# Kernel optimization log

Measured on AMD Instinct MI355X. Metric: run time of the kernel, lower is better.

## Reference

```python
import jax, jax.numpy as jnp
import numpy as np

EMB = 1024
HEADS = 16
BLOCK = 128


def setup_inputs() -> dict:
    key = jax.random.key(0)
    k1, k2, k3 = jax.random.split(key, 3)
    B, T, C = 4, 4096, EMB
    x = jax.random.normal(k1, (B, T, C), dtype=jnp.float32)
    # Linear weights stored as [in, out] (i.e. torch W.T); qkv has no bias.
    W_qkv = jax.random.normal(k2, (C, 3 * C), dtype=jnp.float32) * 0.02
    W_proj = jax.random.normal(k3, (C, C), dtype=jnp.float32) * 0.02
    b_proj = jnp.zeros((C,), dtype=jnp.float32)
    return {"x": x, "W_qkv": W_qkv, "W_proj": W_proj, "b_proj": b_proj}


def reference(x, W_qkv, W_proj, b_proj):
    # Dropout is inference-mode identity.
    B, T, C = x.shape
    H, D, BS = HEADS, C // HEADS, BLOCK
    nb = T // BS  # number of local blocks
    qkv = x @ W_qkv  # [B,T,3C]
    q, k, v = jnp.split(qkv, 3, axis=-1)
    # [B, nb, BS, H, D] -- each block attends only within itself
    q = q.reshape(B, nb, BS, H, D)
    k = k.reshape(B, nb, BS, H, D)
    v = v.reshape(B, nb, BS, H, D)
    scores = jnp.einsum("bnqhd,bnkhd->bnhqk", q, k) / jnp.sqrt(jnp.float32(D))
    # is_decoder: causal tril within each diagonal block (tril[i:end, i:end])
    tril = jnp.tril(jnp.ones((BS, BS), dtype=bool))
    scores = jnp.where(tril, scores, -jnp.inf)
    # faithful to original: stable exp, then divide by (sum + 1e-6)
    scores = scores - jnp.max(scores, axis=-1, keepdims=True)
    e = jnp.exp(scores)
    p = e / (jnp.sum(e, axis=-1, keepdims=True) + 1e-6)
    out = jnp.einsum("bnhqk,bnkhd->bnqhd", p, v).reshape(B, T, C)
    return out @ W_proj + b_proj
```

## Files before the change

### kernel.cpp

```cpp
#include <hip/hip_runtime.h>
#include <hip/hip_bf16.h>
#include <math.h>


typedef __bf16 bf16_t;
typedef __bf16 bf16x8 __attribute__((ext_vector_type(8)));
typedef float  f32x4  __attribute__((ext_vector_type(4)));

typedef const __attribute__((address_space(1))) void* gptr_t;
typedef __attribute__((address_space(3))) void* lptr_t;

__global__ __launch_bounds__(256) void cvt_f32_bf16(const float* __restrict__ in,
                                                    bf16_t* __restrict__ out, size_t n) {
    size_t stride = (size_t)gridDim.x * blockDim.x * 4;
    for (size_t i = ((size_t)blockIdx.x * blockDim.x + threadIdx.x) * 4; i < n; i += stride) {
        float4 v = *(const float4*)(in + i);
        bf16_t t[4];
        t[0] = (bf16_t)v.x; t[1] = (bf16_t)v.y; t[2] = (bf16_t)v.z; t[3] = (bf16_t)v.w;
        *(uint2*)(out + i) = *(uint2*)t;
    }
}

__global__ __launch_bounds__(256) void transpose_cvt(const float* __restrict__ in,
                                                     bf16_t* __restrict__ out, int K, int N) {
    __shared__ float tile[32][33];
    const int tx = threadIdx.x & 31, ty = threadIdx.x >> 5;
    const int bx = blockIdx.x, by = blockIdx.y;
    #pragma unroll
    for (int i = 0; i < 4; i++) {
        const int k = by * 32 + ty + i * 8;
        tile[ty + i * 8][tx] = in[(size_t)k * N + bx * 32 + tx];
    }
    __syncthreads();
    #pragma unroll
    for (int i = 0; i < 4; i++) {
        const int n = bx * 32 + ty + i * 8;
        out[(size_t)n * K + by * 32 + tx] = (bf16_t)tile[tx][ty + i * 8];
    }
}

template <bool BF16_OUT, bool BIAS>
__global__ __launch_bounds__(256) void gemm_bt(const bf16_t* __restrict__ A,
                                               const bf16_t* __restrict__ Bt,
                                               void* __restrict__ Cout,
                                               const float* __restrict__ bias,
                                               int M, int N, int K) {
    __shared__ bf16_t As[2][128 * 32];
    __shared__ bf16_t Bs[2][128 * 32];

    const int bn = blockIdx.x, bm = blockIdx.y;
    const int tid = threadIdx.x;
    const int lane = tid & 63, wave = tid >> 6;
    const int wm = wave >> 1, wn = wave & 1;
    const int quad = lane >> 4, l16 = lane & 15;

    const bf16_t* Ab = A  + (size_t)bm * 128 * K;
    const bf16_t* Bb = Bt + (size_t)bn * 128 * K;

    f32x4 acc[4][4];
    for (int i = 0; i < 4; i++)
        for (int j = 0; j < 4; j++)
            acc[i][j] = (f32x4){0.f, 0.f, 0.f, 0.f};

    const int srow = lane >> 2;
    const int scb  = (lane & 3) * 16;

    for (int k0 = 0; k0 < K; k0 += 64) {
        #pragma unroll
        for (int half = 0; half < 2; half++) {
            #pragma unroll
            for (int i = 0; i < 2; i++) {
                const int s = wave * 2 + i;
                const int row = s * 16 + srow;
                const int kk = k0 + half * 32;
                __builtin_amdgcn_global_load_lds(
                    (gptr_t)((const char*)(Ab + (size_t)row * K + kk) + scb),
                    (lptr_t)&As[half][s * 512], 16, 0, 0);
                __builtin_amdgcn_global_load_lds(
                    (gptr_t)((const char*)(Bb + (size_t)row * K + kk) + scb),
                    (lptr_t)&Bs[half][s * 512], 16, 0, 0);
            }
        }
        __syncthreads();

        #pragma unroll
        for (int half = 0; half < 2; half++) {
            bf16x8 af[4], bf[4];
            #pragma unroll
            for (int mr = 0; mr < 4; mr++)
                af[mr] = *(const bf16x8*)&As[half][(wm * 64 + mr * 16 + l16) * 32 + quad * 8];
            #pragma unroll
            for (int nr = 0; nr < 4; nr++)
                bf[nr] = *(const bf16x8*)&Bs[half][(wn * 64 + nr * 16 + l16) * 32 + quad * 8];
            #pragma unroll
            for (int mr = 0; mr < 4; mr++)
                #pragma unroll
                for (int nr = 0; nr < 4; nr++)
                    acc[mr][nr] = __builtin_amdgcn_mfma_f32_16x16x32_bf16(af[mr], bf[nr], acc[mr][nr], 0, 0, 0);
        }
        __syncthreads();
    }

    #pragma unroll
    for (int mr = 0; mr < 4; mr++) {
        #pragma unroll
        for (int nr = 0; nr < 4; nr++) {
            const int gcol = bn * 128 + wn * 64 + nr * 16 + l16;
            #pragma unroll
            for (int reg = 0; reg < 4; reg++) {
                const int grow = bm * 128 + wm * 64 + mr * 16 + quad * 4 + reg;
                float v = acc[mr][nr][reg];
                if (BIAS) v += bias[gcol];
                if (BF16_OUT)
                    ((bf16_t*)Cout)[(size_t)grow * N + gcol] = (bf16_t)v;
                else
                    ((float*)Cout)[(size_t)grow * N + gcol] = v;
            }
        }
    }
}

__global__ __launch_bounds__(256, 3) void attn_kernel(const bf16_t* __restrict__ qkv,
                                                      bf16_t* __restrict__ attn_out) {
    __shared__ __align__(16) char smem[54272];
    bf16_t* qs = (bf16_t*)smem;
    bf16_t* ks = (bf16_t*)(smem + 18432);
    bf16_t* vT = (bf16_t*)(smem + 36864);
    bf16_t* ps = (bf16_t*)smem;

    const int tid = threadIdx.x;
    const int lane = tid & 63, wave = tid >> 6;
    const int quad = lane >> 4, l16 = lane & 15;

    const int bid = blockIdx.x;
    const int h = bid & 15;
    const int blk = (bid >> 4) & 31;
    const int b = bid >> 9;
    const int row0 = (b * 32 + blk) * 128;
    const int LDQ = 3072;

    for (int t = tid; t < 128 * 8; t += 256) {
        const int r = t >> 3;
        const int c = (t & 7) * 8;
        const bf16_t* src = qkv + (size_t)(row0 + r) * LDQ + h * 64;
        *(uint4*)&qs[r * 72 + c] = *(const uint4*)(src + c);
        *(uint4*)&ks[r * 72 + c] = *(const uint4*)(src + 1024 + c);
        bf16x8 vv = *(const bf16x8*)(src + 2048 + c);
        #pragma unroll
        for (int j = 0; j < 8; j++)
            vT[(c + j) * 136 + r] = vv[j];
    }
    __syncthreads();

    f32x4 sfrag[2][8];
    for (int mr = 0; mr < 2; mr++)
        for (int nc = 0; nc < 8; nc++)
            sfrag[mr][nc] = (f32x4){0.f, 0.f, 0.f, 0.f};

    #pragma unroll
    for (int ksl = 0; ksl < 2; ksl++) {
        bf16x8 aq[2], bk[8];
        #pragma unroll
        for (int mr = 0; mr < 2; mr++)
            aq[mr] = *(const bf16x8*)&qs[(wave * 32 + mr * 16 + l16) * 72 + ksl * 32 + quad * 8];
        #pragma unroll
        for (int nc = 0; nc < 8; nc++)
            bk[nc] = *(const bf16x8*)&ks[(nc * 16 + l16) * 72 + ksl * 32 + quad * 8];
        #pragma unroll
        for (int mr = 0; mr < 2; mr++)
            #pragma unroll
            for (int nc = 0; nc < 8; nc++)
                sfrag[mr][nc] = __builtin_amdgcn_mfma_f32_16x16x32_bf16(aq[mr], bk[nc], sfrag[mr][nc], 0, 0, 0);
    }

    #pragma unroll
    for (int mr = 0; mr < 2; mr++) {
        #pragma unroll
        for (int nc = 0; nc < 8; nc++) {
            #pragma unroll
            for (int reg = 0; reg < 4; reg++) {
                const int row = wave * 32 + mr * 16 + quad * 4 + reg;
                const int col = nc * 16 + l16;
                float s = sfrag[mr][nc][reg] * 0.125f;
                if (col > row) s = -INFINITY;
                sfrag[mr][nc][reg] = s;
            }
        }
    }

    #pragma unroll
    for (int mr = 0; mr < 2; mr++) {
        #pragma unroll
        for (int reg = 0; reg < 4; reg++) {
            float m = -INFINITY;
            #pragma unroll
            for (int nc = 0; nc < 8; nc++) m = fmaxf(m, sfrag[mr][nc][reg]);
            #pragma unroll
            for (int off = 1; off < 16; off <<= 1) m = fmaxf(m, __shfl_xor(m, off));
            float sum = 0.f;
            #pragma unroll
            for (int nc = 0; nc < 8; nc++) {
                float e = __expf(sfrag[mr][nc][reg] - m);
                sfrag[mr][nc][reg] = e;
                sum += e;
            }
            #pragma unroll
            for (int off = 1; off < 16; off <<= 1) sum += __shfl_xor(sum, off);
            const float inv = 1.0f / (sum + 1e-6f);
            #pragma unroll
            for (int nc = 0; nc < 8; nc++) sfrag[mr][nc][reg] *= inv;
        }
    }

    __syncthreads();

    #pragma unroll
    for (int mr = 0; mr < 2; mr++)
        #pragma unroll
        for (int nc = 0; nc < 8; nc++)
            #pragma unroll
            for (int reg = 0; reg < 4; reg++) {
                const int row = wave * 32 + mr * 16 + quad * 4 + reg;
                const int col = nc * 16 + l16;
                ps[row * 136 + col] = (bf16_t)sfrag[mr][nc][reg];
            }
    __syncthreads();

    f32x4 oacc[2][4];
    for (int mr = 0; mr < 2; mr++)
        for (int nd = 0; nd < 4; nd++)
            oacc[mr][nd] = (f32x4){0.f, 0.f, 0.f, 0.f};

    #pragma unroll
    for (int ksl = 0; ksl < 4; ksl++) {
        bf16x8 ap[2];
        #pragma unroll
        for (int mr = 0; mr < 2; mr++)
            ap[mr] = *(const bf16x8*)&ps[(wave * 32 + mr * 16 + l16) * 136 + ksl * 32 + quad * 8];
        #pragma unroll
        for (int nd = 0; nd < 4; nd++) {
            bf16x8 bv = *(const bf16x8*)&vT[(nd * 16 + l16) * 136 + ksl * 32 + quad * 8];
            #pragma unroll
            for (int mr = 0; mr < 2; mr++)
                oacc[mr][nd] = __builtin_amdgcn_mfma_f32_16x16x32_bf16(ap[mr], bv, oacc[mr][nd], 0, 0, 0);
        }
    }

    #pragma unroll
    for (int mr = 0; mr < 2; mr++)
        #pragma unroll
        for (int nd = 0; nd < 4; nd++)
            #pragma unroll
            for (int reg = 0; reg < 4; reg++) {
                const int row = row0 + wave * 32 + mr * 16 + quad * 4 + reg;
                const int col = h * 64 + nd * 16 + l16;
                attn_out[(size_t)row * 1024 + col] = (bf16_t)oacc[mr][nd][reg];
            }
}

extern "C" void kernel_launch(void* const* d_in, const int* in_sizes, int n_in,
                              void* d_out, int out_size, void* d_ws, size_t ws_size,
                              hipStream_t stream) {
    const float* x     = (const float*)d_in[0];
    const float* Wqkv  = (const float*)d_in[1];
    const float* Wproj = (const float*)d_in[2];
    const float* bproj = (const float*)d_in[3];

    const int M = 16384, C = 1024, N1 = 3072;

    char* ws = (char*)d_ws;
    bf16_t* xb     = (bf16_t*)(ws);
    bf16_t* wqkvT  = (bf16_t*)(ws + 33554432);
    bf16_t* wprojT = (bf16_t*)(ws + 39845888);
    bf16_t* qkvb   = (bf16_t*)(ws + 41943040);
    bf16_t* attnb  = (bf16_t*)(ws + 142606336);

    cvt_f32_bf16<<<8192, 256, 0, stream>>>(x, xb, (size_t)M * C);
    transpose_cvt<<<dim3(N1 / 32, C / 32), 256, 0, stream>>>(Wqkv, wqkvT, C, N1);
    transpose_cvt<<<dim3(C / 32, C / 32), 256, 0, stream>>>(Wproj, wprojT, C, C);

    gemm_bt<true, false><<<dim3(N1 / 128, M / 128), 256, 0, stream>>>(
        xb, wqkvT, (void*)qkvb, nullptr, M, N1, C);

    attn_kernel<<<2048, 256, 0, stream>>>(qkvb, attnb);

    gemm_bt<false, true><<<dim3(C / 128, M / 128), 256, 0, stream>>>(
        attnb, wprojT, d_out, bproj, M, C, C);
}
```

Before: 350.7 us.

## Skip causally masked tiles in local attention and balance rows across waves

Each wave now owns two 16-row groups paired as g and 7-g, so causal work is spread evenly across the four waves. The QK^T and PV MFMA loops skip key/value tiles that lie entirely above the causal diagonal. This cuts roughly half of the attention matrix multiplies, at the cost of wave-uniform branching inside unrolled loops. Masked tiles stay at zero, are set to -inf and exp to zero, so the result is unchanged.

```diff
diff --git a/kernel.cpp b/kernel.cpp
--- a/kernel.cpp
+++ b/kernel.cpp
@@ -139,6 +139,9 @@
     const int row0 = (b * 32 + blk) * 128;
     const int LDQ = 3072;
 
+    const int wu = __builtin_amdgcn_readfirstlane(wave);
+    const int g0 = wu, g1 = 7 - wu;
+
     for (int t = tid; t < 128 * 8; t += 256) {
         const int r = t >> 3;
         const int c = (t & 7) * 8;
@@ -159,27 +162,27 @@
 
     #pragma unroll
     for (int ksl = 0; ksl < 2; ksl++) {
-        bf16x8 aq[2], bk[8];
-        #pragma unroll
-        for (int mr = 0; mr < 2; mr++)
-            aq[mr] = *(const bf16x8*)&qs[(wave * 32 + mr * 16 + l16) * 72 + ksl * 32 + quad * 8];
-        #pragma unroll
-        for (int nc = 0; nc < 8; nc++)
-            bk[nc] = *(const bf16x8*)&ks[(nc * 16 + l16) * 72 + ksl * 32 + quad * 8];
-        #pragma unroll
-        for (int mr = 0; mr < 2; mr++)
-            #pragma unroll
-            for (int nc = 0; nc < 8; nc++)
-                sfrag[mr][nc] = __builtin_amdgcn_mfma_f32_16x16x32_bf16(aq[mr], bk[nc], sfrag[mr][nc], 0, 0, 0);
-    }
-
-    #pragma unroll
-    for (int mr = 0; mr < 2; mr++) {
+        bf16x8 aq0 = *(const bf16x8*)&qs[(g0 * 16 + l16) * 72 + ksl * 32 + quad * 8];
+        bf16x8 aq1 = *(const bf16x8*)&qs[(g1 * 16 + l16) * 72 + ksl * 32 + quad * 8];
         #pragma unroll
         for (int nc = 0; nc < 8; nc++) {
+            if (nc <= g1) {
+                bf16x8 bk = *(const bf16x8*)&ks[(nc * 16 + l16) * 72 + ksl * 32 + quad * 8];
+                sfrag[1][nc] = __builtin_amdgcn_mfma_f32_16x16x32_bf16(aq1, bk, sfrag[1][nc], 0, 0, 0);
+                if (nc <= g0)
+                    sfrag[0][nc] = __builtin_amdgcn_mfma_f32_16x16x32_bf16(aq0, bk, sfrag[0][nc], 0, 0, 0);
+            }
+        }
+    }
+
+    #pragma unroll
+    for (int mr = 0; mr < 2; mr++) {
+        const int g = mr ? g1 : g0;
+        #pragma unroll
+        for (int nc = 0; nc < 8; nc++) {
             #pragma unroll
             for (int reg = 0; reg < 4; reg++) {
-                const int row = wave * 32 + mr * 16 + quad * 4 + reg;
+                const int row = g * 16 + quad * 4 + reg;
                 const int col = nc * 16 + l16;
                 float s = sfrag[mr][nc][reg] * 0.125f;
                 if (col > row) s = -INFINITY;
@@ -215,15 +218,15 @@
     __syncthreads();
 
     #pragma unroll
-    for (int mr = 0; mr < 2; mr++)
+    for (int mr = 0; mr < 2; mr++) {
+        const int g = mr ? g1 : g0;
+        const int rbase = g * 16 + quad * 4;
         #pragma unroll
         for (int nc = 0; nc < 8; nc++)
             #pragma unroll
-            for (int reg = 0; reg < 4; reg++) {
-                const int row = wave * 32 + mr * 16 + quad * 4 + reg;
-                const int col = nc * 16 + l16;
-                ps[row * 136 + col] = (bf16_t)sfrag[mr][nc][reg];
-            }
+            for (int reg = 0; reg < 4; reg++)
+                ps[(rbase + reg) * 136 + nc * 16 + l16] = (bf16_t)sfrag[mr][nc][reg];
+    }
     __syncthreads();
 
     f32x4 oacc[2][4];
@@ -231,31 +234,38 @@
         for (int nd = 0; nd < 4; nd++)
             oacc[mr][nd] = (f32x4){0.f, 0.f, 0.f, 0.f};
 
+    const int s0 = g0 >> 1, s1 = g1 >> 1;
     #pragma unroll
     for (int ksl = 0; ksl < 4; ksl++) {
-        bf16x8 ap[2];
-        #pragma unroll
-        for (int mr = 0; mr < 2; mr++)
-            ap[mr] = *(const bf16x8*)&ps[(wave * 32 + mr * 16 + l16) * 136 + ksl * 32 + quad * 8];
+        if (ksl <= s1) {
+            bf16x8 ap1 = *(const bf16x8*)&ps[(g1 * 16 + l16) * 136 + ksl * 32 + quad * 8];
+            bf16x8 ap0;
+            const bool use0 = (ksl <= s0);
+            if (use0)
+                ap0 = *(const bf16x8*)&ps[(g0 * 16 + l16) * 136 + ksl * 32 + quad * 8];
+            #pragma unroll
+            for (int nd = 0; nd < 4; nd++) {
+                bf16x8 bv = *(const bf16x8*)&vT[(nd * 16 + l16) * 136 + ksl * 32 + quad * 8];
+                oacc[1][nd] = __builtin_amdgcn_mfma_f32_16x16x32_bf16(ap1, bv, oacc[1][nd], 0, 0, 0);
+                if (use0)
+                    oacc[0][nd] = __builtin_amdgcn_mfma_f32_16x16x32_bf16(ap0, bv, oacc[0][nd], 0, 0, 0);
+            }
+        }
+    }
+
+    #pragma unroll
+    for (int mr = 0; mr < 2; mr++) {
+        const int g = mr ? g1 : g0;
         #pragma unroll
         for (int nd = 0; nd < 4; nd++) {
-            bf16x8 bv = *(const bf16x8*)&vT[(nd * 16 + l16) * 136 + ksl * 32 + quad * 8];
-            #pragma unroll
-            for (int mr = 0; mr < 2; mr++)
-                oacc[mr][nd] = __builtin_amdgcn_mfma_f32_16x16x32_bf16(ap[mr], bv, oacc[mr][nd], 0, 0, 0);
-        }
-    }
-
-    #pragma unroll
-    for (int mr = 0; mr < 2; mr++)
-        #pragma unroll
-        for (int nd = 0; nd < 4; nd++)
             #pragma unroll
             for (int reg = 0; reg < 4; reg++) {
-                const int row = row0 + wave * 32 + mr * 16 + quad * 4 + reg;
+                const int row = row0 + g * 16 + quad * 4 + reg;
                 const int col = h * 64 + nd * 16 + l16;
                 attn_out[(size_t)row * 1024 + col] = (bf16_t)oacc[mr][nd][reg];
             }
+        }
+    }
 }
 
 extern "C" void kernel_launch(void* const* d_in, const int* in_sizes, int n_in,
```

New measurement: 354.2 us. About the same (+1.0%).
